# Performance work log

Measured on AMD Instinct MI355X. Metric: run time of the kernel, lower is better.

Reference implementation:

```python
import jax, jax.numpy as jnp
import numpy as np

N_NODES = 48758  # hardcoded in the original DAN.forward
EPS_BN = 1e-5


def setup_inputs() -> dict:
    key = jax.random.key(0)
    ks = jax.random.split(key, 14)
    E, D, R, L, NI = 780000, 128, 4, 2, 10000
    sc = 1.0 / np.sqrt(D)
    inp = {
        "x": jax.random.normal(ks[0], (N_NODES, D), jnp.float32),
        "edge_index": jax.random.randint(ks[1], (2, E), 0, N_NODES),
        "idx": jax.random.randint(ks[2], (NI,), 0, N_NODES),
        "edge_type": jax.random.randint(ks[3], (E,), 0, R),
        "edge_weight": jax.random.uniform(ks[4], (E,), jnp.float32),
        # RiskGNN params
        "proj_w": jax.random.normal(ks[5], (D, D), jnp.float32) * sc,
        "proj_b": jax.random.normal(ks[6], (D,), jnp.float32) * 0.01,
        "bn_g": jnp.ones((D,), jnp.float32),
        "bn_b": jnp.zeros((D,), jnp.float32),
        # per-layer DAN params, stacked over L=2 layers (same dims)
        "win_w": jax.random.normal(ks[7], (L, D, D), jnp.float32) * sc,
        "win_b": jax.random.normal(ks[8], (L, D), jnp.float32) * 0.01,
        "wrel": jax.random.normal(ks[9], (L, R, D, D), jnp.float32) * sc,
        "out_w": jax.random.normal(ks[10], (L, D, D), jnp.float32) * sc,
        "out_b": jax.random.normal(ks[11], (L, D), jnp.float32) * 0.01,
    }
    return inp


def _dan_layer(h, edge_index, edge_type, rel_num, win_w, win_b, wrel, out_w, out_b):
    dst = edge_index[0]
    src = edge_index[1]
    x = h @ win_w + win_b                       # [N, D]
    x_j = x[src]                                # edge gather [E, D]
    # gcn_norm(add_self_loops=False): deg over col (=src axis edge_index[1])
    ones_e = jnp.ones(dst.shape[0], x.dtype)
    deg = jax.ops.segment_sum(ones_e, src, num_segments=N_NODES)
    dinv = jnp.where(deg > 0, jax.lax.rsqrt(jnp.maximum(deg, 1.0)), 0.0)
    norm_w = (dinv[dst] * dinv[src])[:, None]   # [E, 1]
    msg_gcn = jax.ops.segment_sum(x_j * norm_w, dst, num_segments=N_NODES)
    # per-relation masked matmul (unsorted grouped GEMM)
    res = jnp.zeros_like(x_j)
    for r in range(rel_num):
        res = jnp.where((edge_type == r)[:, None], x_j @ wrel[r], res)
    # segment softmax over edges grouped by dst, per channel
    seg_max = jax.ops.segment_max(res, dst, num_segments=N_NODES)
    ex = jnp.exp(res - seg_max[dst])
    denom = jax.ops.segment_sum(ex, dst, num_segments=N_NODES)
    weig = ex / denom[dst]
    msg = jax.ops.segment_sum(res * weig, dst, num_segments=N_NODES)
    out = (msg_gcn + 0.1 * jax.nn.relu(msg)) @ out_w + out_b
    return out


def reference(x, edge_weight, proj_w, proj_b, bn_g, bn_b, win_w, win_b, wrel,
              out_w, out_b, edge_index, edge_type, idx):
    rel_num = wrel.shape[1]
    n_layer = win_w.shape[0]
    h = x @ proj_w + proj_b
    # BatchNorm1d (training-mode batch stats, biased var)
    mu = jnp.mean(h, axis=0)
    var = jnp.mean((h - mu) ** 2, axis=0)
    h = (h - mu) * jax.lax.rsqrt(var + EPS_BN) * bn_g + bn_b
    h = jax.nn.relu(h)
    for i in range(n_layer):
        h = _dan_layer(h, edge_index, edge_type, rel_num,
                       win_w[i], win_b[i], wrel[i], out_w[i], out_b[i])
    h = jax.nn.gelu(h, approximate=False)  # dropout is identity at eval
    return h[idx]
```

## Files before the change

kernel.cpp:

```cpp
#include <hip/hip_runtime.h>
#include <hip/hip_bf16.h>
#include <math.h>

#define D 128
#define DD (128 * 128)
#define BCAP 6600

typedef __attribute__((ext_vector_type(8))) short short8;
typedef __attribute__((ext_vector_type(4))) float f32x4;

__device__ __forceinline__ float bf2f(unsigned short u) {
    union { unsigned int i; float f; } x; x.i = ((unsigned int)u) << 16; return x.f;
}
__device__ __forceinline__ unsigned short f2bf(float f) {
    unsigned int i = __float_as_uint(f);
    unsigned int r = (i + 0x7FFFu + ((i >> 16) & 1u)) >> 16;
    return (unsigned short)r;
}

__device__ __forceinline__ int vote_flag(const unsigned short* __restrict__ x) {
    __shared__ int bad_s;
    if (threadIdx.x == 0) bad_s = 0;
    __syncthreads();
    unsigned int e = (x[threadIdx.x] >> 7) & 0xFFu;
    unsigned long long b = __ballot(e < 100u || e > 140u);
    if ((threadIdx.x & 63) == 0) atomicAdd(&bad_s, __popcll(b));
    __syncthreads();
    return bad_s > 48 ? 1 : 0;
}

__global__ __launch_bounds__(256) void k_normall(
    const void* __restrict__ xin, unsigned short* __restrict__ xb, int n4, int nbx,
    const void* s0, const void* s1, const void* s2, const void* s3,
    const void* s4, const void* s5, const void* s6, const void* s7, const void* s8,
    int o1, int o2, int o3, int o4, int o5, int o6, int o7, int o8,
    int total, unsigned short* __restrict__ wdst)
{
    int fl = vote_flag((const unsigned short*)xin);
    if (blockIdx.x < nbx) {
        int i = blockIdx.x * 256 + threadIdx.x;
        if (i >= n4) return;
        if (fl) {
            float4 v = ((const float4*)xin)[i];
            uint2 o;
            o.x = (unsigned int)f2bf(v.x) | ((unsigned int)f2bf(v.y) << 16);
            o.y = (unsigned int)f2bf(v.z) | ((unsigned int)f2bf(v.w) << 16);
            ((uint2*)xb)[i] = o;
        } else {
            ((uint2*)xb)[i] = ((const uint2*)xin)[i];
        }
    } else {
        int i = (blockIdx.x - nbx) * 256 + threadIdx.x;
        if (i >= total) return;
        const void* src; int base;
        if      (i < o1) { src = s0; base = 0;  }
        else if (i < o2) { src = s1; base = o1; }
        else if (i < o3) { src = s2; base = o2; }
        else if (i < o4) { src = s3; base = o3; }
        else if (i < o5) { src = s4; base = o4; }
        else if (i < o6) { src = s5; base = o5; }
        else if (i < o7) { src = s6; base = o6; }
        else if (i < o8) { src = s7; base = o7; }
        else             { src = s8; base = o8; }
        int li = i - base;
        wdst[i] = fl ? f2bf(((const float*)src)[li]) : ((const unsigned short*)src)[li];
    }
}

__device__ __forceinline__ void gemm_core(
    const unsigned short* __restrict__ A, const unsigned short* __restrict__ W,
    int M, int blockRow, unsigned short* As, unsigned short* Wt, f32x4 (&acc)[2][8])
{
    int t = threadIdx.x;
    #pragma unroll
    for (int i = 0; i < 8; ++i) {
        int ch = t + i * 256;
        int row = ch >> 4;
        int kc  = ch & 15;
        int grow = blockRow + row;
        uint4 v = make_uint4(0u, 0u, 0u, 0u);
        if (grow < M) v = *((const uint4*)(A + (size_t)grow * D + kc * 8));
        int kcs = kc ^ (row & 15);
        *((uint4*)&As[row * 128 + kcs * 8]) = v;
    }
    #pragma unroll
    for (int i = 0; i < 8; ++i) {
        int ch = t + i * 256;
        int k  = ch >> 4;
        int n0 = (ch & 15) * 8;
        uint4 v = *((const uint4*)(W + k * D + n0));
        const unsigned short* pv = (const unsigned short*)&v;
        int kc = k >> 3;
        int ko = k & 7;
        #pragma unroll
        for (int j = 0; j < 8; ++j) {
            int n = n0 + j;
            Wt[n * 128 + ((kc ^ (n & 15)) * 8) + ko] = pv[j];
        }
    }
    __syncthreads();

    int wave = t >> 6, lane = t & 63, quad = lane >> 4, l16 = lane & 15;
    int rowbase = wave * 32;

    #pragma unroll
    for (int a = 0; a < 2; ++a)
        #pragma unroll
        for (int b = 0; b < 8; ++b) acc[a][b] = (f32x4){0.f, 0.f, 0.f, 0.f};

    #pragma unroll
    for (int ks = 0; ks < 4; ++ks) {
        int chunk = ks * 4 + quad;
        short8 af[2];
        short8 bf[8];
        #pragma unroll
        for (int rt = 0; rt < 2; ++rt) {
            int r = rowbase + rt * 16 + l16;
            af[rt] = *((const short8*)&As[r * 128 + (chunk ^ (r & 15)) * 8]);
        }
        #pragma unroll
        for (int ct = 0; ct < 8; ++ct) {
            int n = ct * 16 + l16;
            bf[ct] = *((const short8*)&Wt[n * 128 + (chunk ^ (n & 15)) * 8]);
        }
        #pragma unroll
        for (int rt = 0; rt < 2; ++rt)
            #pragma unroll
            for (int ct = 0; ct < 8; ++ct)
                acc[rt][ct] = __builtin_amdgcn_mfma_f32_16x16x32_bf16(af[rt], bf[ct], acc[rt][ct], 0, 0, 0);
    }
}

__device__ __forceinline__ void store_c(
    f32x4 (&acc)[2][8], const unsigned short* __restrict__ bias,
    unsigned short* __restrict__ C, int M, int blockRow, int ldc, int coloff)
{
    int t = threadIdx.x;
    int wave = t >> 6, lane = t & 63, quad = lane >> 4, l16 = lane & 15;
    int rowbase = wave * 32;
    #pragma unroll
    for (int rt = 0; rt < 2; ++rt) {
        #pragma unroll
        for (int ct = 0; ct < 8; ++ct) {
            int col = ct * 16 + l16;
            float bv = bias ? bf2f(bias[col]) : 0.f;
            #pragma unroll
            for (int r = 0; r < 4; ++r) {
                int grow = blockRow + rowbase + rt * 16 + quad * 4 + r;
                if (grow < M) {
                    float v = acc[rt][ct][r] + bv;
                    C[(size_t)grow * ldc + coloff + col] = f2bf(v);
                }
            }
        }
    }
}

__global__ __launch_bounds__(256) void gemm_compose(
    const unsigned short* __restrict__ w_in, const unsigned short* __restrict__ wrel,
    const unsigned short* __restrict__ b_in, unsigned short* __restrict__ wc,
    unsigned short* __restrict__ bc)
{
    __shared__ unsigned short As[DD];
    __shared__ unsigned short Wt[DD];
    f32x4 acc[2][8];
    int b = blockIdx.x;
    int l = b >> 2;
    const unsigned short* A = w_in + (size_t)l * DD;
    const unsigned short* W = wrel + (size_t)b * DD;
    gemm_core(A, W, 128, 0, As, Wt, acc);
    store_c(acc, nullptr, wc + (size_t)b * DD, 128, 0, D, 0);
    int t = threadIdx.x;
    if (t < 128) {
        float s = 0.f;
        for (int k = 0; k < 128; ++k)
            s += bf2f(b_in[l * D + k]) * bf2f(W[k * D + t]);
        bc[b * D + t] = f2bf(s);
    }
}

__global__ __launch_bounds__(256) void k_prepw(
    const unsigned short* __restrict__ wbase, const unsigned short* __restrict__ wc,
    unsigned short* __restrict__ wtg, int o4, int o7)
{
    int m = blockIdx.x >> 3;
    int sub = blockIdx.x & 7;
    const unsigned short* src;
    if (m == 0)       src = wbase;
    else if (m <= 2)  src = wbase + o4 + (m - 1) * DD;
    else if (m <= 10) src = wc + (size_t)(m - 3) * DD;
    else              src = wbase + o7 + (m - 11) * DD;
    int c = sub * 256 + threadIdx.x;
    int n = c >> 4;
    int kc = c & 15;
    unsigned short tmp[8];
    #pragma unroll
    for (int ko = 0; ko < 8; ++ko) tmp[ko] = src[(kc * 8 + ko) * 128 + n];
    *((uint4*)(wtg + (size_t)m * DD + n * 128 + ((kc ^ (n & 15)) * 8))) = *(uint4*)tmp;
}

__device__ __forceinline__ void gemm_core_fast(
    const unsigned short* __restrict__ A,
    const unsigned short* __restrict__ Wt_g,
    int M, int blockRow, unsigned short* Wt, f32x4 (&acc)[2][8])
{
    int t = threadIdx.x;
    #pragma unroll
    for (int i = 0; i < 8; ++i)
        ((uint4*)Wt)[t + i * 256] = ((const uint4*)Wt_g)[t + i * 256];

    int wave = t >> 6, lane = t & 63, quad = lane >> 4, l16 = lane & 15;
    int rowbase = blockRow + wave * 32;
    int r0 = min(rowbase + l16, M - 1);
    int r1 = min(rowbase + 16 + l16, M - 1);
    const unsigned short* a0 = A + (size_t)r0 * D;
    const unsigned short* a1 = A + (size_t)r1 * D;
    short8 af[2][4];
    #pragma unroll
    for (int ks = 0; ks < 4; ++ks) {
        int chunk = ks * 4 + quad;
        af[0][ks] = *((const short8*)(a0 + chunk * 8));
        af[1][ks] = *((const short8*)(a1 + chunk * 8));
    }
    #pragma unroll
    for (int a = 0; a < 2; ++a)
        #pragma unroll
        for (int b = 0; b < 8; ++b) acc[a][b] = (f32x4){0.f, 0.f, 0.f, 0.f};
    __syncthreads();
    #pragma unroll
    for (int ks = 0; ks < 4; ++ks) {
        int chunk = ks * 4 + quad;
        short8 bf[8];
        #pragma unroll
        for (int ct = 0; ct < 8; ++ct)
            bf[ct] = *((const short8*)&Wt[(ct * 16 + l16) * 128 + ((chunk ^ l16) * 8)]);
        #pragma unroll
        for (int rt = 0; rt < 2; ++rt)
            #pragma unroll
            for (int ct = 0; ct < 8; ++ct)
                acc[rt][ct] = __builtin_amdgcn_mfma_f32_16x16x32_bf16(af[rt][ks], bf[ct], acc[rt][ct], 0, 0, 0);
    }
}

__global__ __launch_bounds__(256) void gemm_fast(
    const unsigned short* __restrict__ A, const unsigned short* __restrict__ Wt_g,
    const unsigned short* __restrict__ bias, unsigned short* __restrict__ C,
    int M, int ldc, int coloff)
{
    __shared__ unsigned short Wt[DD];
    f32x4 acc[2][8];
    gemm_core_fast(A, Wt_g, M, blockIdx.x * 128, Wt, acc);
    store_c(acc, bias, C, M, blockIdx.x * 128, ldc, coloff);
}

__global__ __launch_bounds__(256) void gemm_proj(
    const unsigned short* __restrict__ A, const unsigned short* __restrict__ Wt_g,
    const unsigned short* __restrict__ bias, unsigned short* __restrict__ C,
    int M, float* __restrict__ psum, float* __restrict__ psq)
{
    __shared__ unsigned short Wt[DD];
    __shared__ float smS[4][128], smQ[4][128];
    f32x4 acc[2][8];
    int blockRow = blockIdx.x * 128;
    gemm_core_fast(A, Wt_g, M, blockRow, Wt, acc);

    int t = threadIdx.x;
    int wave = t >> 6, lane = t & 63, quad = lane >> 4, l16 = lane & 15;
    int rowbase = wave * 32;
    #pragma unroll
    for (int ct = 0; ct < 8; ++ct) {
        int col = ct * 16 + l16;
        float bv = bf2f(bias[col]);
        float ps = 0.f, pq = 0.f;
        #pragma unroll
        for (int rt = 0; rt < 2; ++rt) {
            #pragma unroll
            for (int r = 0; r < 4; ++r) {
                int grow = blockRow + rowbase + rt * 16 + quad * 4 + r;
                if (grow < M) {
                    float v = acc[rt][ct][r] + bv;
                    C[(size_t)grow * D + col] = f2bf(v);
                    ps += v; pq += v * v;
                }
            }
        }
        ps += __shfl_xor(ps, 16, 64); ps += __shfl_xor(ps, 32, 64);
        pq += __shfl_xor(pq, 16, 64); pq += __shfl_xor(pq, 32, 64);
        if (quad == 0) { smS[wave][col] = ps; smQ[wave][col] = pq; }
    }
    __syncthreads();
    if (t < 128) {
        float s = smS[0][t] + smS[1][t] + smS[2][t] + smS[3][t];
        float q = smQ[0][t] + smQ[1][t] + smQ[2][t] + smQ[3][t];
        psum[blockIdx.x * 128 + t] = s;
        psq[blockIdx.x * 128 + t] = q;
    }
}

__global__ __launch_bounds__(256) void gemm_fused(
    const unsigned short* __restrict__ h, const unsigned short* __restrict__ wtg,
    const unsigned short* __restrict__ b_in_l, const unsigned short* __restrict__ bc_l,
    unsigned short* __restrict__ xl, unsigned short* __restrict__ y,
    const float* __restrict__ dinv, int M, int l)
{
    __shared__ unsigned short Wt[DD];
    f32x4 acc[2][8];
    int slice = blockIdx.y;
    int m = (slice == 0) ? (1 + l) : (3 + l * 4 + slice - 1);
    int blockRow = blockIdx.x * 128;
    gemm_core_fast(h, wtg + (size_t)m * DD, M, blockRow, Wt, acc);
    int t = threadIdx.x;
    int wave = t >> 6, lane = t & 63, quad = lane >> 4, l16 = lane & 15;
    int rowbase = wave * 32;
    if (slice == 0) {
        const unsigned short* bias = b_in_l;
        #pragma unroll
        for (int rt = 0; rt < 2; ++rt) {
            float dv[4];
            #pragma unroll
            for (int r = 0; r < 4; ++r) {
                int grow = min(blockRow + rowbase + rt * 16 + quad * 4 + r, M - 1);
                dv[r] = dinv[grow];
            }
            #pragma unroll
            for (int ct = 0; ct < 8; ++ct) {
                int col = ct * 16 + l16;
                float bv = bf2f(bias[col]);
                #pragma unroll
                for (int r = 0; r < 4; ++r) {
                    int grow = blockRow + rowbase + rt * 16 + quad * 4 + r;
                    if (grow < M)
                        xl[(size_t)grow * D + col] = f2bf((acc[rt][ct][r] + bv) * dv[r]);
                }
            }
        }
    } else {
        store_c(acc, bc_l + (slice - 1) * D, y, M, blockRow, 4 * D, (slice - 1) * D);
    }
}

__global__ __launch_bounds__(256) void gemm_out(
    const unsigned short* __restrict__ zg, const unsigned short* __restrict__ Wt_g,
    const unsigned short* __restrict__ bias, void* __restrict__ out,
    int M, const unsigned short* __restrict__ xprobe)
{
    int fl = vote_flag(xprobe);
    __shared__ unsigned short Wt[DD];
    f32x4 acc[2][8];
    int blockRow = blockIdx.x * 128;
    gemm_core_fast(zg, Wt_g, M, blockRow, Wt, acc);
    int t = threadIdx.x;
    int wave = t >> 6, lane = t & 63, quad = lane >> 4, l16 = lane & 15;
    int rowbase = wave * 32;
    #pragma unroll
    for (int rt = 0; rt < 2; ++rt) {
        #pragma unroll
        for (int ct = 0; ct < 8; ++ct) {
            int col = ct * 16 + l16;
            float bv = bf2f(bias[col]);
            #pragma unroll
            for (int r = 0; r < 4; ++r) {
                int grow = blockRow + rowbase + rt * 16 + quad * 4 + r;
                if (grow < M) {
                    float v = acc[rt][ct][r] + bv;
                    float gl = 0.5f * v * (1.f + erff(v * 0.70710678118654752f));
                    size_t o = (size_t)grow * D + col;
                    if (fl) ((float*)out)[o] = gl;
                    else    ((unsigned short*)out)[o] = f2bf(gl);
                }
            }
        }
    }
}

__global__ __launch_bounds__(256) void k_hista(
    const int* __restrict__ ei, int E,
    unsigned int* __restrict__ part_dst, unsigned int* __restrict__ part_src)
{
    __shared__ unsigned int hd[256], hs[256];
    int b = blockIdx.x, t = threadIdx.x;
    hd[t] = 0u; hs[t] = 0u;
    __syncthreads();
    int base = b * 2048;
    #pragma unroll
    for (int i = 0; i < 8; ++i) {
        int e = base + t + i * 256;
        if (e < E) {
            atomicAdd(&hd[((unsigned int)ei[e]) >> 8], 1u);
            atomicAdd(&hs[((unsigned int)ei[E + e]) >> 8], 1u);
        }
    }
    __syncthreads();
    part_dst[b * 256 + t] = hd[t];
    part_src[b * 256 + t] = hs[t];
}

__global__ void k_scanpart(unsigned int* __restrict__ part_d, unsigned int* __restrict__ part_s,
                           unsigned int* __restrict__ btot_d, unsigned int* __restrict__ btot_s,
                           int BA)
{
    __shared__ unsigned int arr[512];
    unsigned int* part = blockIdx.y ? part_s : part_d;
    unsigned int* btot = blockIdx.y ? btot_s : btot_d;
    int bucket = blockIdx.x, t = threadIdx.x;
    unsigned int v0 = (t < BA) ? part[t * 256 + bucket] : 0u;
    unsigned int v1 = (t + 256 < BA) ? part[(t + 256) * 256 + bucket] : 0u;
    arr[t] = v0; arr[t + 256] = v1;
    __syncthreads();
    for (int off = 1; off < 512; off <<= 1) {
        unsigned int a = arr[t], b2 = arr[t + 256];
        unsigned int pa = (t >= off) ? arr[t - off] : 0u;
        unsigned int pb = (t + 256 >= off) ? arr[t + 256 - off] : 0u;
        __syncthreads();
        arr[t] = a + pa; arr[t + 256] = b2 + pb;
        __syncthreads();
    }
    if (t < BA) part[t * 256 + bucket] = arr[t] - v0;
    if (t + 256 < BA) part[(t + 256) * 256 + bucket] = arr[t + 256] - v1;
    if (t == 0) btot[bucket] = arr[511];
}

__global__ void k_scanbase(const unsigned int* __restrict__ btot_d, const unsigned int* __restrict__ btot_s,
                           unsigned int* __restrict__ bbase_d, unsigned int* __restrict__ bbase_s)
{
    __shared__ unsigned int a1[256], a2[256];
    int t = threadIdx.x;
    unsigned int vd = btot_d[t], vs = btot_s[t];
    a1[t] = vd; a2[t] = vs;
    __syncthreads();
    for (int off = 1; off < 256; off <<= 1) {
        unsigned int x = a1[t], y = a2[t];
        unsigned int px = (t >= off) ? a1[t - off] : 0u;
        unsigned int py = (t >= off) ? a2[t - off] : 0u;
        __syncthreads();
        a1[t] = x + px; a2[t] = y + py;
        __syncthreads();
    }
    bbase_d[t] = a1[t] - vd;
    bbase_s[t] = a2[t] - vs;
    if (t == 255) { bbase_d[256] = a1[255]; bbase_s[256] = a2[255]; }
}

__global__ __launch_bounds__(256) void k_bscatter(
    const int* __restrict__ ei, const int* __restrict__ et, int E,
    const unsigned int* __restrict__ part_dst, const unsigned int* __restrict__ part_src,
    const unsigned int* __restrict__ bbase_d, const unsigned int* __restrict__ bbase_s,
    uint2* __restrict__ ebuck, unsigned short* __restrict__ sbuck)
{
    __shared__ unsigned int cd[256], cs[256];
    int b = blockIdx.x, t = threadIdx.x;
    cd[t] = part_dst[b * 256 + t] + bbase_d[t];
    cs[t] = part_src[b * 256 + t] + bbase_s[t];
    __syncthreads();
    int base = b * 2048;
    #pragma unroll
    for (int i = 0; i < 8; ++i) {
        int e = base + t + i * 256;
        if (e < E) {
            unsigned int d = (unsigned int)ei[e];
            unsigned int s = (unsigned int)ei[E + e];
            unsigned int tt = (unsigned int)et[e];
            unsigned int pd = atomicAdd(&cd[d >> 8], 1u);
            ebuck[pd] = make_uint2(d, s | (tt << 16));
            unsigned int ps = atomicAdd(&cs[s >> 8], 1u);
            sbuck[ps] = (unsigned short)s;
        }
    }
}

__global__ __launch_bounds__(256) void k_buckets(
    const unsigned int* __restrict__ bbase_d, const uint2* __restrict__ ebuck,
    unsigned int* __restrict__ rp, unsigned int* __restrict__ pckd,
    const unsigned int* __restrict__ bbase_s, const unsigned short* __restrict__ sbuck,
    float* __restrict__ dinv, int N)
{
    __shared__ uint2 ebuf[BCAP];
    __shared__ unsigned int bins[256], scn[256], cur[256];
    int b = blockIdx.x, t = threadIdx.x;
    if (blockIdx.y == 0) {
        unsigned int beg = bbase_d[b], end = bbase_d[b + 1];
        unsigned int cnt = end - beg;
        bins[t] = 0u;
        __syncthreads();
        bool fit = cnt <= (unsigned int)BCAP;
        if (fit) {
            for (unsigned int i = t; i < cnt; i += 256) {
                uint2 v = ebuck[beg + i];
                ebuf[i] = v;
                atomicAdd(&bins[v.x & 255u], 1u);
            }
        } else {
            for (unsigned int i = t; i < cnt; i += 256)
                atomicAdd(&bins[ebuck[beg + i].x & 255u], 1u);
        }
        __syncthreads();
        scn[t] = bins[t];
        __syncthreads();
        for (int off = 1; off < 256; off <<= 1) {
            unsigned int v = scn[t];
            unsigned int a = (t >= off) ? scn[t - off] : 0u;
            __syncthreads();
            scn[t] = v + a;
            __syncthreads();
        }
        unsigned int ex = scn[t] - bins[t];
        int n = (b << 8) + t;
        if (n <= N) rp[n] = beg + ex;
        cur[t] = beg + ex;
        __syncthreads();
        if (fit) {
            for (unsigned int i = t; i < cnt; i += 256) {
                uint2 v = ebuf[i];
                unsigned int pos = atomicAdd(&cur[v.x & 255u], 1u);
                pckd[pos] = v.y;
            }
        } else {
            for (unsigned int i = t; i < cnt; i += 256) {
                uint2 v = ebuck[beg + i];
                unsigned int pos = atomicAdd(&cur[v.x & 255u], 1u);
                pckd[pos] = v.y;
            }
        }
    } else {
        unsigned int beg = bbase_s[b], end = bbase_s[b + 1];
        bins[t] = 0u;
        __syncthreads();
        for (unsigned int i = beg + t; i < end; i += 256)
            atomicAdd(&bins[sbuck[i] & 255u], 1u);
        __syncthreads();
        int n = (b << 8) + t;
        if (n < N) {
            unsigned int dg = bins[t];
            dinv[n] = dg ? rsqrtf((float)dg) : 0.f;
        }
    }
}

__global__ void k_bnstats(const float* __restrict__ psum, const float* __restrict__ psq,
                          int nb, int N, const unsigned short* __restrict__ g,
                          const unsigned short* __restrict__ b,
                          float* __restrict__ scale, float* __restrict__ shift) {
    int col = threadIdx.x & 127, h = threadIdx.x >> 7;
    float s = 0.f, q = 0.f;
    for (int i = h; i < nb; i += 2) { s += psum[i * 128 + col]; q += psq[i * 128 + col]; }
    __shared__ float sS[256], sQ[256];
    sS[threadIdx.x] = s; sQ[threadIdx.x] = q;
    __syncthreads();
    if (h == 0) {
        s = sS[col] + sS[col + 128];
        q = sQ[col] + sQ[col + 128];
        float inv = 1.f / (float)N;
        float mean = s * inv;
        float var = fmaxf(q * inv - mean * mean, 0.f);
        float sc = rsqrtf(var + 1e-5f) * bf2f(g[col]);
        scale[col] = sc;
        shift[col] = bf2f(b[col]) - mean * sc;
    }
}

__global__ void k_bnrelu(unsigned short* __restrict__ h, const float* __restrict__ scale,
                         const float* __restrict__ shift, int n8) {
    int i = blockIdx.x * blockDim.x + threadIdx.x;
    if (i >= n8) return;
    int cb = (i & 15) * 8;
    uint4 v = ((uint4*)h)[i];
    unsigned int* w = (unsigned int*)&v;
    #pragma unroll
    for (int j = 0; j < 4; ++j) {
        int c = cb + j * 2;
        float v0 = __uint_as_float(w[j] << 16);
        float v1 = __uint_as_float(w[j] & 0xFFFF0000u);
        v0 = fmaxf(fmaf(v0, scale[c], shift[c]), 0.f);
        v1 = fmaxf(fmaf(v1, scale[c + 1], shift[c + 1]), 0.f);
        w[j] = (unsigned int)f2bf(v0) | ((unsigned int)f2bf(v1) << 16);
    }
    ((uint4*)h)[i] = v;
}

__device__ __forceinline__ void acc_edge(uint4 xv, uint4 yv, float vm,
                                         float* g, float* dd, float* ss) {
    const unsigned int* xw = (const unsigned int*)&xv;
    const unsigned int* yw = (const unsigned int*)&yv;
    #pragma unroll
    for (int w = 0; w < 4; ++w) {
        float x0 = __uint_as_float(xw[w] << 16);
        float x1 = __uint_as_float(xw[w] & 0xFFFF0000u);
        float v0 = __uint_as_float(yw[w] << 16);
        float v1 = __uint_as_float(yw[w] & 0xFFFF0000u);
        int j0 = 2 * w, j1 = 2 * w + 1;
        g[j0] = fmaf(x0, vm, g[j0]);
        g[j1] = fmaf(x1, vm, g[j1]);
        float e0 = __expf(v0), e1 = __expf(v1);
        dd[j0] = fmaf(e0, vm, dd[j0]);
        dd[j1] = fmaf(e1, vm, dd[j1]);
        ss[j0] = fmaf(v0 * e0, vm, ss[j0]);
        ss[j1] = fmaf(v1 * e1, vm, ss[j1]);
    }
}

__global__ __launch_bounds__(256) void k_edge(
    const unsigned int* __restrict__ rp, const unsigned int* __restrict__ packed,
    const unsigned short* __restrict__ xl, const unsigned short* __restrict__ y,
    const float* __restrict__ dinv, unsigned short* __restrict__ zout,
    int NN, int RD, const int* __restrict__ nodes)
{
    int lane = threadIdx.x & 63;
    int slot = blockIdx.x * 4 + (threadIdx.x >> 6);
    if (slot >= NN) return;
    int node = nodes ? nodes[slot] : slot;
    node = __builtin_amdgcn_readfirstlane(node);
    unsigned int beg = rp[node], end = rp[node + 1];
    int eg = lane >> 4;
    int cb = (lane & 15) * 8;
    float g[8], dd[8], ss[8];
    #pragma unroll
    for (int j = 0; j < 8; ++j) { g[j] = 0.f; dd[j] = 0.f; ss[j] = 0.f; }

    for (unsigned int e0 = beg; e0 < end; e0 += 8) {
        unsigned int eA = e0 + (unsigned int)eg;
        unsigned int eB = eA + 4u;
        float vmA = (eA < end) ? 1.f : 0.f;
        float vmB = (eB < end) ? 1.f : 0.f;
        unsigned int pA = packed[(eA < end) ? eA : beg];
        unsigned int pB = packed[(eB < end) ? eB : beg];
        unsigned int sA = pA & 0xFFFFu, tA = pA >> 16;
        unsigned int sB = pB & 0xFFFFu, tB = pB >> 16;
        uint4 xvA = *((const uint4*)(xl + (size_t)sA * D + cb));
        uint4 yvA = *((const uint4*)(y + (size_t)sA * RD + tA * D + cb));
        uint4 xvB = *((const uint4*)(xl + (size_t)sB * D + cb));
        uint4 yvB = *((const uint4*)(y + (size_t)sB * RD + tB * D + cb));
        acc_edge(xvA, yvA, vmA, g, dd, ss);
        acc_edge(xvB, yvB, vmB, g, dd, ss);
    }

    #pragma unroll
    for (int j = 0; j < 8; ++j) {
        g[j]  += __shfl_xor(g[j], 16, 64);  g[j]  += __shfl_xor(g[j], 32, 64);
        dd[j] += __shfl_xor(dd[j], 16, 64); dd[j] += __shfl_xor(dd[j], 32, 64);
        ss[j] += __shfl_xor(ss[j], 16, 64); ss[j] += __shfl_xor(ss[j], 32, 64);
    }
    if (eg == 0) {
        float dn = dinv[node];
        unsigned int o[4];
        #pragma unroll
        for (int w = 0; w < 4; ++w) {
            int j0 = w * 2, j1 = w * 2 + 1;
            float m0 = (dd[j0] > 0.f) ? ss[j0] / dd[j0] : 0.f;
            float m1 = (dd[j1] > 0.f) ? ss[j1] / dd[j1] : 0.f;
            float z0 = fmaf(g[j0], dn, 0.1f * fmaxf(m0, 0.f));
            float z1 = fmaf(g[j1], dn, 0.1f * fmaxf(m1, 0.f));
            o[w] = (unsigned int)f2bf(z0) | ((unsigned int)f2bf(z1) << 16);
        }
        *((uint4*)(zout + (size_t)slot * D + cb)) = *(uint4*)o;
    }
}

extern "C" void kernel_launch(void* const* d_in, const int* in_sizes, int n_in,
                              void* d_out, int out_size, void* d_ws, size_t ws_size,
                              hipStream_t stream)
{
    const int* ei  = (const int*)d_in[1];
    const int* idx = (const int*)d_in[2];
    const int* et  = (const int*)d_in[3];
    const unsigned short* xprobe = (const unsigned short*)d_in[0];

    int N  = in_sizes[0] / D;
    int E  = in_sizes[1] / 2;
    int NI = in_sizes[2];
    int L  = in_sizes[9] / (D * D);
    int R  = in_sizes[11] / (L * D * D);
    int RD = R * D;

    int NB = (N + 255) >> 8;
    int BA = (E + 2047) / 2048;

    char* ws = (char*)d_ws;
    size_t off = 0;
    auto alloc = [&](size_t bytes) -> char* {
        char* p = ws + off;
        off += (bytes + 255) & ~(size_t)255;
        return p;
    };
    unsigned short* h    = (unsigned short*)alloc((size_t)N * D * 2);
    unsigned short* xl   = (unsigned short*)alloc((size_t)N * D * 2);
    unsigned short* y    = (unsigned short*)alloc((size_t)N * RD * 2);
    unsigned short* z    = (unsigned short*)alloc((size_t)N * D * 2);
    unsigned short* xb   = (unsigned short*)alloc((size_t)N * D * 2);
    unsigned short* zg   = (unsigned short*)alloc((size_t)NI * D * 2);
    float*          dinv = (float*)alloc((size_t)N * 4);
    unsigned int*   rp   = (unsigned int*)alloc((size_t)(N + 1) * 4);
    unsigned int*   pckd = (unsigned int*)alloc((size_t)E * 4);
    int gb  = (N + 127) / 128;
    float*          psum = (float*)alloc((size_t)gb * 128 * 4);
    float*          psq  = (float*)alloc((size_t)gb * 128 * 4);
    float*          bscale = (float*)alloc(128 * 4);
    float*          bshift = (float*)alloc(128 * 4);
    unsigned int*   part_dst = (unsigned int*)alloc((size_t)BA * 256 * 4);
    unsigned int*   part_src = (unsigned int*)alloc((size_t)BA * 256 * 4);
    unsigned int*   btot_d   = (unsigned int*)alloc(256 * 4);
    unsigned int*   btot_s   = (unsigned int*)alloc(256 * 4);
    unsigned int*   bbase_d  = (unsigned int*)alloc(257 * 4);
    unsigned int*   bbase_s  = (unsigned int*)alloc(257 * 4);
    uint2*          ebuck = (uint2*)y;
    unsigned short* sbuck = (unsigned short*)z;
    int o1 = D * D;
    int o2 = o1 + D;
    int o3 = o2 + D;
    int o4 = o3 + D;
    int o5 = o4 + L * D * D;
    int o6 = o5 + L * D;
    int o7 = o6 + L * R * D * D;
    int o8 = o7 + L * D * D;
    int wt = o8 + L * D;
    unsigned short* wbase  = (unsigned short*)alloc((size_t)wt * 2);
    unsigned short* b_proj = wbase + o1;
    unsigned short* g_bn   = wbase + o2;
    unsigned short* b_bn   = wbase + o3;
    unsigned short* w_in   = wbase + o4;
    unsigned short* b_in   = wbase + o5;
    unsigned short* w_rel  = wbase + o6;
    unsigned short* b_out  = wbase + o8;
    unsigned short* wc     = (unsigned short*)alloc((size_t)L * R * D * D * 2);
    unsigned short* bc     = (unsigned short*)alloc((size_t)L * R * D * 2);
    unsigned short* wtg    = (unsigned short*)alloc((size_t)13 * DD * 2);
    (void)ws_size; (void)n_in; (void)out_size;

    int gb2 = (NI + 127) / 128;
    int nb4 = (N + 3) / 4;
    int ni4 = (NI + 3) / 4;

    int n4 = N * D / 4;
    int nbx = (n4 + 255) / 256;
    int nbw = (wt + 255) / 256;
    k_normall<<<nbx + nbw, 256, 0, stream>>>(
        d_in[0], xb, n4, nbx,
        d_in[5], d_in[6], d_in[7], d_in[8], d_in[9], d_in[10], d_in[11], d_in[12], d_in[13],
        o1, o2, o3, o4, o5, o6, o7, o8, wt, wbase);

    k_hista<<<BA, 256, 0, stream>>>(ei, E, part_dst, part_src);
    k_scanpart<<<dim3(256, 2), 256, 0, stream>>>(part_dst, part_src, btot_d, btot_s, BA);
    k_scanbase<<<1, 256, 0, stream>>>(btot_d, btot_s, bbase_d, bbase_s);
    k_bscatter<<<BA, 256, 0, stream>>>(ei, et, E, part_dst, part_src, bbase_d, bbase_s, ebuck, sbuck);
    k_buckets<<<dim3(NB, 2), 256, 0, stream>>>(bbase_d, ebuck, rp, pckd, bbase_s, sbuck, dinv, N);

    gemm_compose<<<L * R, 256, 0, stream>>>(w_in, w_rel, b_in, wc, bc);
    k_prepw<<<13 * 8, 256, 0, stream>>>(wbase, wc, wtg, o4, o7);

    gemm_proj<<<gb, 256, 0, stream>>>(xb, wtg, b_proj, h, N, psum, psq);
    k_bnstats<<<1, 256, 0, stream>>>(psum, psq, gb, N, g_bn, b_bn, bscale, bshift);
    int n8 = N * D / 8;
    k_bnrelu<<<(n8 + 255) / 256, 256, 0, stream>>>(h, bscale, bshift, n8);

    gemm_fused<<<dim3(gb, 1 + R), 256, 0, stream>>>(h, wtg, b_in, bc, xl, y, dinv, N, 0);
    k_edge<<<nb4, 256, 0, stream>>>(rp, pckd, xl, y, dinv, z, N, RD, nullptr);
    gemm_fast<<<gb, 256, 0, stream>>>(z, wtg + (size_t)11 * DD, b_out, h, N, D, 0);

    gemm_fused<<<dim3(gb, 1 + R), 256, 0, stream>>>(h, wtg, b_in + D, bc + R * D, xl, y, dinv, N, 1);
    k_edge<<<ni4, 256, 0, stream>>>(rp, pckd, xl, y, dinv, zg, NI, RD, idx);

    gemm_out<<<gb2, 256, 0, stream>>>(zg, wtg + (size_t)12 * DD, b_out + D, d_out, NI, xprobe);
}
```

Baseline: 382.8 us.

## Sort edges by relation, split y per relation, batch fused GEMM slices, unroll edge loop

The edge bucketing now sorts edges within each destination by (dst, relation), so a node's edges that share a relation are read together. The relation-projected tensor y moves from node-major [N,R*D] to relation-major [R,N,D]. The fused input GEMM keeps the A fragment in registers and loops over 2-3 weight slices per block instead of launching one block per slice. The edge aggregation loop is unrolled to four edges per iteration with predicated loads, and the masked fma for the GCN sum becomes a plain add because masked lanes now load zeros. BCAP is reduced slightly for the larger shared bin array, which adds more shared-memory scan work per bucket and trades GEMM parallelism for register reuse.

```diff
diff --git a/kernel.cpp b/kernel.cpp
--- a/kernel.cpp
+++ b/kernel.cpp
@@ -4,7 +4,7 @@
 
 #define D 128
 #define DD (128 * 128)
-#define BCAP 6600
+#define BCAP 6400
 
 typedef __attribute__((ext_vector_type(8))) short short8;
 typedef __attribute__((ext_vector_type(4))) float f32x4;
@@ -199,34 +199,32 @@
     *((uint4*)(wtg + (size_t)m * DD + n * 128 + ((kc ^ (n & 15)) * 8))) = *(uint4*)tmp;
 }
 
-__device__ __forceinline__ void gemm_core_fast(
-    const unsigned short* __restrict__ A,
-    const unsigned short* __restrict__ Wt_g,
-    int M, int blockRow, unsigned short* Wt, f32x4 (&acc)[2][8])
+__device__ __forceinline__ void load_afrag(
+    const unsigned short* __restrict__ A, int M, int blockRow, short8 (&af)[2][4])
 {
     int t = threadIdx.x;
-    #pragma unroll
-    for (int i = 0; i < 8; ++i)
-        ((uint4*)Wt)[t + i * 256] = ((const uint4*)Wt_g)[t + i * 256];
-
     int wave = t >> 6, lane = t & 63, quad = lane >> 4, l16 = lane & 15;
     int rowbase = blockRow + wave * 32;
     int r0 = min(rowbase + l16, M - 1);
     int r1 = min(rowbase + 16 + l16, M - 1);
     const unsigned short* a0 = A + (size_t)r0 * D;
     const unsigned short* a1 = A + (size_t)r1 * D;
-    short8 af[2][4];
     #pragma unroll
     for (int ks = 0; ks < 4; ++ks) {
         int chunk = ks * 4 + quad;
         af[0][ks] = *((const short8*)(a0 + chunk * 8));
         af[1][ks] = *((const short8*)(a1 + chunk * 8));
     }
+}
+
+__device__ __forceinline__ void mfma_slice(
+    const unsigned short* Wt, short8 (&af)[2][4], f32x4 (&acc)[2][8])
+{
+    int lane = threadIdx.x & 63, quad = lane >> 4, l16 = lane & 15;
     #pragma unroll
     for (int a = 0; a < 2; ++a)
         #pragma unroll
         for (int b = 0; b < 8; ++b) acc[a][b] = (f32x4){0.f, 0.f, 0.f, 0.f};
-    __syncthreads();
     #pragma unroll
     for (int ks = 0; ks < 4; ++ks) {
         int chunk = ks * 4 + quad;
@@ -240,6 +238,21 @@
             for (int ct = 0; ct < 8; ++ct)
                 acc[rt][ct] = __builtin_amdgcn_mfma_f32_16x16x32_bf16(af[rt][ks], bf[ct], acc[rt][ct], 0, 0, 0);
     }
+}
+
+__device__ __forceinline__ void gemm_core_fast(
+    const unsigned short* __restrict__ A,
+    const unsigned short* __restrict__ Wt_g,
+    int M, int blockRow, unsigned short* Wt, f32x4 (&acc)[2][8])
+{
+    int t = threadIdx.x;
+    #pragma unroll
+    for (int i = 0; i < 8; ++i)
+        ((uint4*)Wt)[t + i * 256] = ((const uint4*)Wt_g)[t + i * 256];
+    short8 af[2][4];
+    load_afrag(A, M, blockRow, af);
+    __syncthreads();
+    mfma_slice(Wt, af, acc);
 }
 
 __global__ __launch_bounds__(256) void gemm_fast(
@@ -297,45 +310,56 @@
     }
 }
 
-__global__ __launch_bounds__(256) void gemm_fused(
+__global__ __launch_bounds__(256) void gemm_fused5(
     const unsigned short* __restrict__ h, const unsigned short* __restrict__ wtg,
     const unsigned short* __restrict__ b_in_l, const unsigned short* __restrict__ bc_l,
     unsigned short* __restrict__ xl, unsigned short* __restrict__ y,
-    const float* __restrict__ dinv, int M, int l)
+    const float* __restrict__ dinv, int M, int Ntot, int l)
 {
     __shared__ unsigned short Wt[DD];
-    f32x4 acc[2][8];
-    int slice = blockIdx.y;
-    int m = (slice == 0) ? (1 + l) : (3 + l * 4 + slice - 1);
+    int t = threadIdx.x;
     int blockRow = blockIdx.x * 128;
-    gemm_core_fast(h, wtg + (size_t)m * DD, M, blockRow, Wt, acc);
-    int t = threadIdx.x;
+    short8 af[2][4];
+    load_afrag(h, M, blockRow, af);
+    int s0 = (blockIdx.y == 0) ? 0 : 2;
+    int s1 = (blockIdx.y == 0) ? 2 : 5;
     int wave = t >> 6, lane = t & 63, quad = lane >> 4, l16 = lane & 15;
     int rowbase = wave * 32;
-    if (slice == 0) {
-        const unsigned short* bias = b_in_l;
-        #pragma unroll
-        for (int rt = 0; rt < 2; ++rt) {
-            float dv[4];
+    for (int slice = s0; slice < s1; ++slice) {
+        int m = (slice == 0) ? (1 + l) : (3 + l * 4 + slice - 1);
+        const unsigned short* Wt_g = wtg + (size_t)m * DD;
+        #pragma unroll
+        for (int i = 0; i < 8; ++i)
+            ((uint4*)Wt)[t + i * 256] = ((const uint4*)Wt_g)[t + i * 256];
+        __syncthreads();
+        f32x4 acc[2][8];
+        mfma_slice(Wt, af, acc);
+        if (slice == 0) {
             #pragma unroll
-            for (int r = 0; r < 4; ++r) {
-                int grow = min(blockRow + rowbase + rt * 16 + quad * 4 + r, M - 1);
-                dv[r] = dinv[grow];
-            }
-            #pragma unroll
-            for (int ct = 0; ct < 8; ++ct) {
-                int col = ct * 16 + l16;
-                float bv = bf2f(bias[col]);
+            for (int rt = 0; rt < 2; ++rt) {
+                float dv[4];
                 #pragma unroll
                 for (int r = 0; r < 4; ++r) {
-                    int grow = blockRow + rowbase + rt * 16 + quad * 4 + r;
-                    if (grow < M)
-                        xl[(size_t)grow * D + col] = f2bf((acc[rt][ct][r] + bv) * dv[r]);
+                    int grow = min(blockRow + rowbase + rt * 16 + quad * 4 + r, M - 1);
+                    dv[r] = dinv[grow];
+                }
+                #pragma unroll
+                for (int ct = 0; ct < 8; ++ct) {
+                    int col = ct * 16 + l16;
+                    float bv = bf2f(b_in_l[col]);
+                    #pragma unroll
+                    for (int r = 0; r < 4; ++r) {
+                        int grow = blockRow + rowbase + rt * 16 + quad * 4 + r;
+                        if (grow < M)
+                            xl[(size_t)grow * D + col] = f2bf((acc[rt][ct][r] + bv) * dv[r]);
+                    }
                 }
             }
-        }
-    } else {
-        store_c(acc, bc_l + (slice - 1) * D, y, M, blockRow, 4 * D, (slice - 1) * D);
+        } else {
+            store_c(acc, bc_l + (slice - 1) * D, y + (size_t)(slice - 1) * Ntot * D,
+                    M, blockRow, D, 0);
+        }
+        __syncthreads();
     }
 }
 
@@ -475,49 +499,59 @@
     float* __restrict__ dinv, int N)
 {
     __shared__ uint2 ebuf[BCAP];
-    __shared__ unsigned int bins[256], scn[256], cur[256];
+    __shared__ unsigned int bins[1024], gsum[256];
     int b = blockIdx.x, t = threadIdx.x;
     if (blockIdx.y == 0) {
         unsigned int beg = bbase_d[b], end = bbase_d[b + 1];
         unsigned int cnt = end - beg;
-        bins[t] = 0u;
+        #pragma unroll
+        for (int j = 0; j < 4; ++j) bins[t + j * 256] = 0u;
         __syncthreads();
         bool fit = cnt <= (unsigned int)BCAP;
         if (fit) {
             for (unsigned int i = t; i < cnt; i += 256) {
                 uint2 v = ebuck[beg + i];
                 ebuf[i] = v;
-                atomicAdd(&bins[v.x & 255u], 1u);
+                atomicAdd(&bins[((v.x & 255u) << 2) | ((v.y >> 16) & 3u)], 1u);
             }
         } else {
-            for (unsigned int i = t; i < cnt; i += 256)
-                atomicAdd(&bins[ebuck[beg + i].x & 255u], 1u);
-        }
-        __syncthreads();
-        scn[t] = bins[t];
+            for (unsigned int i = t; i < cnt; i += 256) {
+                uint2 v = ebuck[beg + i];
+                atomicAdd(&bins[((v.x & 255u) << 2) | ((v.y >> 16) & 3u)], 1u);
+            }
+        }
+        __syncthreads();
+        unsigned int b0 = bins[4 * t], b1 = bins[4 * t + 1], b2 = bins[4 * t + 2], b3 = bins[4 * t + 3];
+        unsigned int s4 = b0 + b1 + b2 + b3;
+        gsum[t] = s4;
         __syncthreads();
         for (int off = 1; off < 256; off <<= 1) {
-            unsigned int v = scn[t];
-            unsigned int a = (t >= off) ? scn[t - off] : 0u;
+            unsigned int v = gsum[t];
+            unsigned int a = (t >= off) ? gsum[t - off] : 0u;
             __syncthreads();
-            scn[t] = v + a;
+            gsum[t] = v + a;
             __syncthreads();
         }
-        unsigned int ex = scn[t] - bins[t];
+        unsigned int base0 = gsum[t] - s4;
+        bins[4 * t]     = base0;
+        bins[4 * t + 1] = base0 + b0;
+        bins[4 * t + 2] = base0 + b0 + b1;
+        bins[4 * t + 3] = base0 + b0 + b1 + b2;
         int n = (b << 8) + t;
-        if (n <= N) rp[n] = beg + ex;
-        cur[t] = beg + ex;
+        if (n <= N) rp[n] = beg + base0;
         __syncthreads();
         if (fit) {
             for (unsigned int i = t; i < cnt; i += 256) {
                 uint2 v = ebuf[i];
-                unsigned int pos = atomicAdd(&cur[v.x & 255u], 1u);
+                unsigned int key = ((v.x & 255u) << 2) | ((v.y >> 16) & 3u);
+                unsigned int pos = beg + atomicAdd(&bins[key], 1u);
                 pckd[pos] = v.y;
             }
         } else {
             for (unsigned int i = t; i < cnt; i += 256) {
                 uint2 v = ebuck[beg + i];
-                unsigned int pos = atomicAdd(&cur[v.x & 255u], 1u);
+                unsigned int key = ((v.x & 255u) << 2) | ((v.y >> 16) & 3u);
+                unsigned int pos = beg + atomicAdd(&bins[key], 1u);
                 pckd[pos] = v.y;
             }
         }
@@ -588,8 +622,8 @@
         float v0 = __uint_as_float(yw[w] << 16);
         float v1 = __uint_as_float(yw[w] & 0xFFFF0000u);
         int j0 = 2 * w, j1 = 2 * w + 1;
-        g[j0] = fmaf(x0, vm, g[j0]);
-        g[j1] = fmaf(x1, vm, g[j1]);
+        g[j0] += x0;
+        g[j1] += x1;
         float e0 = __expf(v0), e1 = __expf(v1);
         dd[j0] = fmaf(e0, vm, dd[j0]);
         dd[j1] = fmaf(e1, vm, dd[j1]);
@@ -602,7 +636,7 @@
     const unsigned int* __restrict__ rp, const unsigned int* __restrict__ packed,
     const unsigned short* __restrict__ xl, const unsigned short* __restrict__ y,
     const float* __restrict__ dinv, unsigned short* __restrict__ zout,
-    int NN, int RD, const int* __restrict__ nodes)
+    int NN, int Ntot, const int* __restrict__ nodes)
 {
     int lane = threadIdx.x & 63;
     int slot = blockIdx.x * 4 + (threadIdx.x >> 6);
@@ -616,21 +650,26 @@
     #pragma unroll
     for (int j = 0; j < 8; ++j) { g[j] = 0.f; dd[j] = 0.f; ss[j] = 0.f; }
 
-    for (unsigned int e0 = beg; e0 < end; e0 += 8) {
-        unsigned int eA = e0 + (unsigned int)eg;
-        unsigned int eB = eA + 4u;
-        float vmA = (eA < end) ? 1.f : 0.f;
-        float vmB = (eB < end) ? 1.f : 0.f;
-        unsigned int pA = packed[(eA < end) ? eA : beg];
-        unsigned int pB = packed[(eB < end) ? eB : beg];
-        unsigned int sA = pA & 0xFFFFu, tA = pA >> 16;
-        unsigned int sB = pB & 0xFFFFu, tB = pB >> 16;
-        uint4 xvA = *((const uint4*)(xl + (size_t)sA * D + cb));
-        uint4 yvA = *((const uint4*)(y + (size_t)sA * RD + tA * D + cb));
-        uint4 xvB = *((const uint4*)(xl + (size_t)sB * D + cb));
-        uint4 yvB = *((const uint4*)(y + (size_t)sB * RD + tB * D + cb));
-        acc_edge(xvA, yvA, vmA, g, dd, ss);
-        acc_edge(xvB, yvB, vmB, g, dd, ss);
+    for (unsigned int e0 = beg; e0 < end; e0 += 16) {
+        uint4 xv[4], yv[4];
+        float vm[4];
+        #pragma unroll
+        for (int u = 0; u < 4; ++u) {
+            unsigned int e = e0 + u * 4 + (unsigned int)eg;
+            bool valid = e < end;
+            vm[u] = valid ? 1.f : 0.f;
+            xv[u] = make_uint4(0u, 0u, 0u, 0u);
+            yv[u] = make_uint4(0u, 0u, 0u, 0u);
+            if (valid) {
+                unsigned int p = packed[e];
+                unsigned int s = p & 0xFFFFu;
+                unsigned int tt = (p >> 16) & 3u;
+                xv[u] = *((const uint4*)(xl + (size_t)s * D + cb));
+                yv[u] = *((const uint4*)(y + ((size_t)tt * Ntot + s) * D + cb));
+            }
+        }
+        #pragma unroll
+        for (int u = 0; u < 4; ++u) acc_edge(xv[u], yv[u], vm[u], g, dd, ss);
     }
 
     #pragma unroll
@@ -669,7 +708,6 @@
     int NI = in_sizes[2];
     int L  = in_sizes[9] / (D * D);
     int R  = in_sizes[11] / (L * D * D);
-    int RD = R * D;
 
     int NB = (N + 255) >> 8;
     int BA = (E + 2047) / 2048;
@@ -683,7 +721,7 @@
     };
     unsigned short* h    = (unsigned short*)alloc((size_t)N * D * 2);
     unsigned short* xl   = (unsigned short*)alloc((size_t)N * D * 2);
-    unsigned short* y    = (unsigned short*)alloc((size_t)N * RD * 2);
+    unsigned short* y    = (unsigned short*)alloc((size_t)N * R * D * 2);
     unsigned short* z    = (unsigned short*)alloc((size_t)N * D * 2);
     unsigned short* xb   = (unsigned short*)alloc((size_t)N * D * 2);
     unsigned short* zg   = (unsigned short*)alloc((size_t)NI * D * 2);
@@ -751,12 +789,12 @@
     int n8 = N * D / 8;
     k_bnrelu<<<(n8 + 255) / 256, 256, 0, stream>>>(h, bscale, bshift, n8);
 
-    gemm_fused<<<dim3(gb, 1 + R), 256, 0, stream>>>(h, wtg, b_in, bc, xl, y, dinv, N, 0);
-    k_edge<<<nb4, 256, 0, stream>>>(rp, pckd, xl, y, dinv, z, N, RD, nullptr);
+    gemm_fused5<<<dim3(gb, 2), 256, 0, stream>>>(h, wtg, b_in, bc, xl, y, dinv, N, N, 0);
+    k_edge<<<nb4, 256, 0, stream>>>(rp, pckd, xl, y, dinv, z, N, N, nullptr);
     gemm_fast<<<gb, 256, 0, stream>>>(z, wtg + (size_t)11 * DD, b_out, h, N, D, 0);
 
-    gemm_fused<<<dim3(gb, 1 + R), 256, 0, stream>>>(h, wtg, b_in + D, bc + R * D, xl, y, dinv, N, 1);
-    k_edge<<<ni4, 256, 0, stream>>>(rp, pckd, xl, y, dinv, zg, NI, RD, idx);
+    gemm_fused5<<<dim3(gb, 2), 256, 0, stream>>>(h, wtg, b_in + D, bc + R * D, xl, y, dinv, N, N, 1);
+    k_edge<<<ni4, 256, 0, stream>>>(rp, pckd, xl, y, dinv, zg, NI, N, idx);
 
     gemm_out<<<gb2, 256, 0, stream>>>(zg, wtg + (size_t)12 * DD, b_out + D, d_out, NI, xprobe);
 }
```

New measurement: 411.6 us. +7.5%, slower.
